# Kernel tuning notes

Hardware: AMD Instinct MI355X
Metric: run time of the kernel (lower is better)

## Reference

```python
import jax, jax.numpy as jnp
import numpy as np

N_HEAD = 16

def _rope_cos_sin(T, head_dim, dtype):
    # inv_freq over even indices, freqs [T, head_dim//2]
    inv_freq = 1.0 / (10000.0 ** (jnp.arange(0, head_dim, 2, dtype=jnp.float32) / head_dim))
    t = jnp.arange(T, dtype=jnp.float32)
    freqs = t[:, None] * inv_freq[None, :]
    cos = jnp.cos(freqs).astype(dtype)[None, :, None, :]  # [1,T,1,hd/2]
    sin = jnp.sin(freqs).astype(dtype)[None, :, None, :]
    return cos, sin

def _apply_rope(x, cos, sin):
    # x: [B,T,H,hd]; interleaved halves as in the torch module
    x1, x2 = x[..., ::2], x[..., 1::2]
    return jnp.concatenate([x1 * cos - x2 * sin, x1 * sin + x2 * cos], axis=-1)

def setup_inputs() -> dict:
    key = jax.random.key(0)
    k1, k2, k3 = jax.random.split(key, 3)
    B, T, C = 2, 2048, 1024
    x = jax.random.normal(k1, (B, T, C), dtype=jnp.float32)
    # causal mask (mask==0 positions get -inf), broadcast over B and heads
    attn_mask = jnp.tril(jnp.ones((T, T), dtype=bool))[None, None, :, :]
    w_qkv = jax.random.normal(k2, (C, 3 * C), dtype=jnp.float32) * (1.0 / np.sqrt(C))
    w_out = jax.random.normal(k3, (C, C), dtype=jnp.float32) * (1.0 / np.sqrt(C))
    return {"x": x, "attn_mask": attn_mask, "w_qkv": w_qkv, "w_out": w_out}

def reference(x, attn_mask, w_qkv, w_out):
    B, T, C = x.shape
    H = N_HEAD
    hd = C // H
    qkv = x @ w_qkv  # [B,T,3C]
    q, k, v = jnp.split(qkv, 3, axis=2)
    q = q.reshape(B, T, H, hd)
    k = k.reshape(B, T, H, hd)
    v = v.reshape(B, T, H, hd)
    cos, sin = _rope_cos_sin(T, hd, x.dtype)
    q = _apply_rope(q, cos, sin)
    k = _apply_rope(k, cos, sin)
    scale = 1.0 / np.sqrt(hd).astype(np.float32)
    att = jnp.einsum('bthd,bshd->bhts', q, k) * scale  # [B,H,T,T]
    att = jnp.where(attn_mask, att, -jnp.inf)
    att = jax.nn.softmax(att, axis=-1)
    out = jnp.einsum('bhts,bshd->bthd', att, v).reshape(B, T, C)
    out = out @ w_out
    k_t = jnp.transpose(k, (0, 2, 1, 3))  # [B,H,T,hd]
    v_t = jnp.transpose(v, (0, 2, 1, 3))
    return out, k_t, v_t
```

## Files before the change

### kernel.cpp

```cpp
#include <hip/hip_runtime.h>

#define T_SEQ 2048
#define NH    16
#define HD    64
#define CDIM  1024
#define BDIM  2

using floatx4 = __attribute__((ext_vector_type(4))) float;
using bf16x8  = __attribute__((ext_vector_type(8))) __bf16;
using half4   = __attribute__((ext_vector_type(4))) _Float16;
using half8   = __attribute__((ext_vector_type(8))) _Float16;
typedef unsigned short u16;

__device__ __forceinline__ u16 f2bf(float f) {
  unsigned int u = __float_as_uint(f);
  u += 0x7fffu + ((u >> 16) & 1u);
  return (u16)(u >> 16);
}
__device__ __forceinline__ float bf2f(u16 h) {
  return __uint_as_float(((unsigned int)h) << 16);
}
__device__ __forceinline__ u16 f2h(float f) {
  union { _Float16 h; u16 u; } c; c.h = (_Float16)f; return c.u;
}
__device__ __forceinline__ unsigned pk2h(float a, float b) {
  return __builtin_bit_cast(unsigned, __builtin_amdgcn_cvt_pkrtz(a, b));
}
__device__ __forceinline__ void gld16(const void* g, const void* l) {
  __builtin_amdgcn_global_load_lds(
      (const __attribute__((address_space(1))) unsigned int*)(unsigned long long)g,
      (__attribute__((address_space(3))) unsigned int*)(unsigned int)(unsigned long long)l,
      16, 0, 0);
}

__global__ __launch_bounds__(256) void preproc(const float* __restrict__ x,
                                               const float* __restrict__ w_qkv,
                                               const float* __restrict__ w_out,
                                               u16* __restrict__ xb,
                                               u16* __restrict__ wqT,
                                               u16* __restrict__ woT) {
  __shared__ float tile[32][33];
  int blk = blockIdx.x, tid = threadIdx.x;
  if (blk < 4096) {
    int i = blk * 256 + tid;
    float4 v = ((const float4*)x)[i];
    ushort4 o;
    o.x = f2bf(v.x); o.y = f2bf(v.y); o.z = f2bf(v.z); o.w = f2bf(v.w);
    ((ushort4*)xb)[i] = o;
    return;
  }
  const float* W; u16* WT; int K, N, bx, by;
  if (blk < 4096 + 3072) {
    int idx = blk - 4096; W = w_qkv; WT = wqT; K = 1024; N = 3072;
    bx = idx % 96; by = idx / 96;
  } else {
    int idx = blk - 7168; W = w_out; WT = woT; K = 1024; N = 1024;
    bx = idx & 31; by = idx >> 5;
  }
  int n0 = bx * 32, k0 = by * 32;
  int tx = tid & 31, ty = tid >> 5;
#pragma unroll
  for (int i = 0; i < 32; i += 8)
    tile[ty + i][tx] = W[(size_t)(k0 + ty + i) * N + n0 + tx];
  __syncthreads();
#pragma unroll
  for (int i = 0; i < 32; i += 8)
    WT[(size_t)(n0 + ty + i) * K + k0 + tx] = f2bf(tile[tx][ty + i]);
}

template <bool OUT_F32>
__global__ __launch_bounds__(256) void gemm_bt(const u16* __restrict__ A,
                                               const u16* __restrict__ BT,
                                               float* __restrict__ Cf,
                                               u16* __restrict__ Cb,
                                               int M, int N, int K) {
  __shared__ u16 As[128 * 32];
  __shared__ u16 Bs[128 * 32];
  const int tid  = threadIdx.x;
  const int lane = tid & 63, wave = tid >> 6;
  const int quad = lane >> 4, l16 = lane & 15;
  const int wm = (wave & 1) * 64, wn = (wave >> 1) * 64;
  const int row0 = blockIdx.x * 128, col0 = blockIdx.y * 128;
  const int srow = tid >> 2;
  const int sc   = tid & 3;
  const int sgc  = (sc ^ ((srow >> 1) & 3)) * 8;
  floatx4 acc[4][4] = {};
  for (int k0 = 0; k0 < K; k0 += 32) {
    __syncthreads();
    gld16(A  + (size_t)(row0 + srow     ) * K + k0 + sgc, &As[srow * 32 + sc * 8]);
    gld16(A  + (size_t)(row0 + srow + 64) * K + k0 + sgc, &As[(srow + 64) * 32 + sc * 8]);
    gld16(BT + (size_t)(col0 + srow     ) * K + k0 + sgc, &Bs[srow * 32 + sc * 8]);
    gld16(BT + (size_t)(col0 + srow + 64) * K + k0 + sgc, &Bs[(srow + 64) * 32 + sc * 8]);
    __syncthreads();
    bf16x8 af[4], bfv[4];
#pragma unroll
    for (int mt = 0; mt < 4; mt++) {
      int r = wm + mt * 16 + l16;
      af[mt] = *(const bf16x8*)&As[r * 32 + (quad ^ ((r >> 1) & 3)) * 8];
    }
#pragma unroll
    for (int nt = 0; nt < 4; nt++) {
      int r = wn + nt * 16 + l16;
      bfv[nt] = *(const bf16x8*)&Bs[r * 32 + (quad ^ ((r >> 1) & 3)) * 8];
    }
#pragma unroll
    for (int mt = 0; mt < 4; mt++)
#pragma unroll
      for (int nt = 0; nt < 4; nt++)
        acc[mt][nt] = __builtin_amdgcn_mfma_f32_16x16x32_bf16(af[mt], bfv[nt], acc[mt][nt], 0, 0, 0);
  }
#pragma unroll
  for (int mt = 0; mt < 4; mt++)
#pragma unroll
    for (int nt = 0; nt < 4; nt++)
#pragma unroll
      for (int r = 0; r < 4; r++) {
        int row = row0 + wm + mt * 16 + quad * 4 + r;
        int col = col0 + wn + nt * 16 + l16;
        float v = acc[mt][nt][r];
        if (OUT_F32) Cf[(size_t)row * N + col] = v;
        else         Cb[(size_t)row * N + col] = f2bf(v);
      }
}

__global__ __launch_bounds__(256) void rope_vpack(const u16* __restrict__ qkv,
                                                  u16* __restrict__ qf16,
                                                  u16* __restrict__ kf16,
                                                  float* __restrict__ kt_out,
                                                  float* __restrict__ vt_out,
                                                  u16* __restrict__ vtf) {
  int blk = blockIdx.x;
  if (blk < 16384) {
    int gid = blk * 4 + (threadIdx.x >> 6);
    int d   = threadIdx.x & 63;
    int t   = gid & (T_SEQ - 1);
    int h   = (gid >> 11) & 15;
    int b   = gid >> 15;
    const u16* qrow = qkv + ((size_t)(b * T_SEQ + t)) * 3072 + h * 64;
    int i = d & 31;
    unsigned int qp = *(const unsigned int*)(qrow + 2 * i);
    unsigned int kp = *(const unsigned int*)(qrow + 1024 + 2 * i);
    float q1 = bf2f((u16)qp), q2 = bf2f((u16)(qp >> 16));
    float k1 = bf2f((u16)kp), k2 = bf2f((u16)(kp >> 16));
    float inv = expf((float)i * -0.28782313662425572f);
    float ang = (float)t * inv;
    float sn = sinf(ang), cs = cosf(ang);
    float qv = (d < 32) ? (q1 * cs - q2 * sn) : (q1 * sn + q2 * cs);
    float kv = (d < 32) ? (k1 * cs - k2 * sn) : (k1 * sn + k2 * cs);
    size_t o = (size_t)gid * 64 + d;
    qf16[o] = f2h(qv * 0.18033688011112042f);
    kf16[o] = f2h(kv);
    kt_out[o] = kv;
    return;
  }
  __shared__ float tile[64][65];
  int b2 = blk - 16384;
  int t0 = (b2 & 31) * 64;
  int bh = b2 >> 5;
  int b = bh >> 4, h = bh & 15;
  int tx = threadIdx.x & 63, ty = threadIdx.x >> 6;
#pragma unroll
  for (int i = ty; i < 64; i += 4) {
    float v = bf2f(qkv[((size_t)(b * T_SEQ + t0 + i)) * 3072 + 2048 + h * 64 + tx]);
    tile[i][tx] = v;
    vt_out[((size_t)bh * T_SEQ + t0 + i) * 64 + tx] = v;
  }
  __syncthreads();
#pragma unroll
  for (int i = ty; i < 64; i += 4)
    vtf[((size_t)bh * 64 + i) * T_SEQ + t0 + tx] = f2h(tile[tx][i]);
}

__global__ __launch_bounds__(256) void attn_fused(const u16* __restrict__ qf16,
                                                  const u16* __restrict__ kf16,
                                                  const u16* __restrict__ vtf,
                                                  u16* __restrict__ Ob) {
  __shared__ u16 Ks[128 * 64];
  __shared__ u16 Vts[64 * 128];
  const int tid = threadIdx.x;
  const int lane = tid & 63, wave = tid >> 6;
  const int quad = lane >> 4, l16 = lane & 15;
  const int qh2 = quad >> 1, ql2 = (quad & 1) * 4;
  const int j   = blockIdx.x >> 5;
  const int bh  = blockIdx.x & 31;
  const int b = bh >> 4, h = bh & 15;

#pragma unroll 1
  for (int s2 = 0; s2 < 2; s2++) {
    const int qt2 = s2 ? j : (31 - j);
    const int tw  = qt2 * 64 + wave * 16;
    const u16* Qg = qf16 + ((size_t)bh * T_SEQ + tw) * HD;
    half8 qfrag[2];
#pragma unroll
    for (int kc = 0; kc < 2; kc++)
      qfrag[kc] = *(const half8*)&Qg[(size_t)l16 * HD + kc * 32 + quad * 8];

    floatx4 oacc[4] = {};
    float mrow = -1e30f, lrow = 0.f;
    const int nkt = (qt2 >> 1) + 1;

    for (int kt = 0; kt < nkt; kt++) {
      __syncthreads();
      const size_t koff = ((size_t)bh * T_SEQ + kt * 128) * HD;
      const u16* Vg = vtf + (size_t)bh * HD * T_SEQ + kt * 128;
#pragma unroll
      for (int jj = 0; jj < 4; jj++) {
        int t2 = jj * 256 + tid;
        int r = t2 >> 3, c = t2 & 7;
        gld16(kf16 + koff + r * HD + (c ^ (r & 7)) * 8, &Ks[t2 * 8]);
      }
#pragma unroll
      for (int jj = 0; jj < 4; jj++) {
        int t2 = jj * 256 + tid;
        int r = t2 >> 4, c = t2 & 15;
        gld16(Vg + (size_t)r * T_SEQ + (c ^ (r & 15)) * 8, &Vts[t2 * 8]);
      }
      __syncthreads();

      floatx4 sacc[8] = {};
#pragma unroll
      for (int kc = 0; kc < 2; kc++)
#pragma unroll
        for (int st = 0; st < 8; st++) {
          int srow = st * 16 + l16;
          half8 ak = *(const half8*)&Ks[srow * 64 + (((kc * 4 + quad) ^ (srow & 7)) * 8)];
          sacc[st] = __builtin_amdgcn_mfma_f32_16x16x32_f16(ak, qfrag[kc], sacc[st], 0, 0, 0);
        }
      if (kt == nkt - 1) {
        int tg = tw + l16;
#pragma unroll
        for (int st = 0; st < 8; st++) {
          int sg = kt * 128 + st * 16 + quad * 4;
#pragma unroll
          for (int r = 0; r < 4; r++)
            if (sg + r > tg) sacc[st][r] = -1e30f;
        }
      }
      {
        floatx4 vm = sacc[0];
#pragma unroll
        for (int st = 1; st < 8; st++) {
          vm[0] = fmaxf(vm[0], sacc[st][0]); vm[1] = fmaxf(vm[1], sacc[st][1]);
          vm[2] = fmaxf(vm[2], sacc[st][2]); vm[3] = fmaxf(vm[3], sacc[st][3]);
        }
        float mx = fmaxf(fmaxf(vm[0], vm[1]), fmaxf(vm[2], vm[3]));
        mx = fmaxf(mx, __shfl_xor(mx, 16));
        mx = fmaxf(mx, __shfl_xor(mx, 32));
        float mnew = fmaxf(mrow, mx);
        float alpha = exp2f(mrow - mnew);
        mrow = mnew;
        floatx4 vs = {0.f, 0.f, 0.f, 0.f};
#pragma unroll
        for (int st = 0; st < 8; st++) {
#pragma unroll
          for (int r = 0; r < 4; r++) sacc[st][r] = exp2f(sacc[st][r] - mnew);
          vs += sacc[st];
        }
        float rs = (vs[0] + vs[1]) + (vs[2] + vs[3]);
        rs += __shfl_xor(rs, 16);
        rs += __shfl_xor(rs, 32);
        lrow = lrow * alpha + rs;
#pragma unroll
        for (int dt = 0; dt < 4; dt++) oacc[dt] *= alpha;
      }
#pragma unroll
      for (int st = 0; st < 8; st++) {
        union { unsigned u[2]; half4 h; } pc;
        pc.u[0] = pk2h(sacc[st][0], sacc[st][1]);
        pc.u[1] = pk2h(sacc[st][2], sacc[st][3]);
        half4 bp = pc.h;
#pragma unroll
        for (int dt = 0; dt < 4; dt++) {
          int drow = dt * 16 + l16;
          half4 av = *(const half4*)&Vts[drow * 128 + (((st * 2 + qh2) ^ (drow & 15)) * 8) + ql2];
          oacc[dt] = __builtin_amdgcn_mfma_f32_16x16x16f16(av, bp, oacc[dt], 0, 0, 0);
        }
      }
    }
    {
      int t = tw + l16;
      float invl = 1.f / lrow;
#pragma unroll
      for (int dt = 0; dt < 4; dt++) {
        int d0 = dt * 16 + quad * 4;
        ushort4 o;
        o.x = f2bf(oacc[dt][0] * invl);
        o.y = f2bf(oacc[dt][1] * invl);
        o.z = f2bf(oacc[dt][2] * invl);
        o.w = f2bf(oacc[dt][3] * invl);
        *(ushort4*)&Ob[((size_t)(b * T_SEQ) + t) * CDIM + h * HD + d0] = o;
      }
    }
  }
}

extern "C" void kernel_launch(void* const* d_in, const int* in_sizes, int n_in,
                              void* d_out, int out_size, void* d_ws, size_t ws_size,
                              hipStream_t stream) {
  const float* x     = (const float*)d_in[0];
  const float* w_qkv = (const float*)d_in[2];
  const float* w_out = (const float*)d_in[3];
  float* out    = (float*)d_out;
  float* kt_out = out + (size_t)BDIM * T_SEQ * CDIM;
  float* vt_out = kt_out + (size_t)BDIM * T_SEQ * CDIM;

  const size_t F = (size_t)4194304;
  char* base = (char*)d_ws;
  u16* xb   = (u16*)base;
  u16* wqT  = xb + F;
  u16* woT  = wqT + (size_t)3145728;
  u16* qkvb = woT + (size_t)1048576;
  u16* qf16 = qkvb + (size_t)3 * F;
  u16* kf16 = qf16 + F;
  u16* vtf  = (u16*)base;
  u16* Ob   = kf16 + F;

  preproc<<<8192, 256, 0, stream>>>(x, w_qkv, w_out, xb, wqT, woT);
  gemm_bt<false><<<dim3(32, 24), 256, 0, stream>>>(xb, wqT, (float*)nullptr, qkvb, 4096, 3072, 1024);
  rope_vpack<<<17408, 256, 0, stream>>>(qkvb, qf16, kf16, kt_out, vt_out, vtf);
  attn_fused<<<512, 256, 0, stream>>>(qf16, kf16, vtf, Ob);
  gemm_bt<true><<<dim3(32, 8), 256, 0, stream>>>(Ob, woT, out, (u16*)nullptr, 4096, 1024, 1024);
}
```

Measured before the change: 221.0 us.

## Process both causal query tiles together sharing K/V tile loads

The attention kernel now handles its two paired query tiles (31-j and j) in one pass over the key/value tiles instead of two sequential passes. Each loaded K/V tile is reused by both query tiles while both are active, and the dual MFMA streams interleave to raise instruction-level parallelism. It also skips the online-softmax rescale when the new max grows by no more than a threshold, and adds a launch-bounds occupancy hint. In exchange, register pressure roughly doubles for the accumulators, which may limit occupancy.

```diff
diff --git a/kernel.cpp b/kernel.cpp
--- a/kernel.cpp
+++ b/kernel.cpp
@@ -171,10 +171,122 @@
     vtf[((size_t)bh * 64 + i) * T_SEQ + t0 + tx] = f2h(tile[tx][i]);
 }
 
-__global__ __launch_bounds__(256) void attn_fused(const u16* __restrict__ qf16,
-                                                  const u16* __restrict__ kf16,
-                                                  const u16* __restrict__ vtf,
-                                                  u16* __restrict__ Ob) {
+__device__ __forceinline__ void qk_dual(const u16* Ks, const half8* qfA, const half8* qfB,
+                                        floatx4 (&sA)[8], floatx4 (&sB)[8],
+                                        int quad, int l16) {
+#pragma unroll
+  for (int kc = 0; kc < 2; kc++)
+#pragma unroll
+    for (int st = 0; st < 8; st++) {
+      int srow = st * 16 + l16;
+      half8 ak = *(const half8*)&Ks[srow * 64 + (((kc * 4 + quad) ^ (srow & 7)) * 8)];
+      sA[st] = __builtin_amdgcn_mfma_f32_16x16x32_f16(ak, qfA[kc], sA[st], 0, 0, 0);
+      sB[st] = __builtin_amdgcn_mfma_f32_16x16x32_f16(ak, qfB[kc], sB[st], 0, 0, 0);
+    }
+}
+__device__ __forceinline__ void qk_single(const u16* Ks, const half8* qfA,
+                                          floatx4 (&sA)[8], int quad, int l16) {
+#pragma unroll
+  for (int kc = 0; kc < 2; kc++)
+#pragma unroll
+    for (int st = 0; st < 8; st++) {
+      int srow = st * 16 + l16;
+      half8 ak = *(const half8*)&Ks[srow * 64 + (((kc * 4 + quad) ^ (srow & 7)) * 8)];
+      sA[st] = __builtin_amdgcn_mfma_f32_16x16x32_f16(ak, qfA[kc], sA[st], 0, 0, 0);
+    }
+}
+__device__ __forceinline__ void apply_mask(floatx4 (&s)[8], int kt, int tw, int quad, int l16) {
+  int tg = tw + l16;
+#pragma unroll
+  for (int st = 0; st < 8; st++) {
+    int sg = kt * 128 + st * 16 + quad * 4;
+#pragma unroll
+    for (int r = 0; r < 4; r++)
+      if (sg + r > tg) s[st][r] = -1e30f;
+  }
+}
+__device__ __forceinline__ void softmax_update(floatx4 (&s)[8], float& mrow, float& lrow,
+                                               floatx4 (&oacc)[4]) {
+  floatx4 vm = s[0];
+#pragma unroll
+  for (int st = 1; st < 8; st++) {
+    vm[0] = fmaxf(vm[0], s[st][0]); vm[1] = fmaxf(vm[1], s[st][1]);
+    vm[2] = fmaxf(vm[2], s[st][2]); vm[3] = fmaxf(vm[3], s[st][3]);
+  }
+  float mx = fmaxf(fmaxf(vm[0], vm[1]), fmaxf(vm[2], vm[3]));
+  mx = fmaxf(mx, __shfl_xor(mx, 16));
+  mx = fmaxf(mx, __shfl_xor(mx, 32));
+  if (!__all(mx <= mrow + 8.f)) {
+    float mnew = fmaxf(mrow, mx);
+    float alpha = exp2f(mrow - mnew);
+    mrow = mnew;
+    lrow *= alpha;
+#pragma unroll
+    for (int dt = 0; dt < 4; dt++) oacc[dt] *= alpha;
+  }
+  floatx4 vs = {0.f, 0.f, 0.f, 0.f};
+#pragma unroll
+  for (int st = 0; st < 8; st++) {
+#pragma unroll
+    for (int r = 0; r < 4; r++) s[st][r] = exp2f(s[st][r] - mrow);
+    vs += s[st];
+  }
+  float rs = (vs[0] + vs[1]) + (vs[2] + vs[3]);
+  rs += __shfl_xor(rs, 16);
+  rs += __shfl_xor(rs, 32);
+  lrow += rs;
+}
+__device__ __forceinline__ void pv_dual(const u16* Vts, const floatx4 (&sA)[8],
+                                        const floatx4 (&sB)[8], floatx4 (&oA)[4],
+                                        floatx4 (&oB)[4], int qh2, int ql2, int l16) {
+#pragma unroll
+  for (int st = 0; st < 8; st++) {
+    union { unsigned u[2]; half4 h; } pa, pb;
+    pa.u[0] = pk2h(sA[st][0], sA[st][1]); pa.u[1] = pk2h(sA[st][2], sA[st][3]);
+    pb.u[0] = pk2h(sB[st][0], sB[st][1]); pb.u[1] = pk2h(sB[st][2], sB[st][3]);
+#pragma unroll
+    for (int dt = 0; dt < 4; dt++) {
+      int drow = dt * 16 + l16;
+      half4 av = *(const half4*)&Vts[drow * 128 + (((st * 2 + qh2) ^ (drow & 15)) * 8) + ql2];
+      oA[dt] = __builtin_amdgcn_mfma_f32_16x16x16f16(av, pa.h, oA[dt], 0, 0, 0);
+      oB[dt] = __builtin_amdgcn_mfma_f32_16x16x16f16(av, pb.h, oB[dt], 0, 0, 0);
+    }
+  }
+}
+__device__ __forceinline__ void pv_single(const u16* Vts, const floatx4 (&sA)[8],
+                                          floatx4 (&oA)[4], int qh2, int ql2, int l16) {
+#pragma unroll
+  for (int st = 0; st < 8; st++) {
+    union { unsigned u[2]; half4 h; } pa;
+    pa.u[0] = pk2h(sA[st][0], sA[st][1]); pa.u[1] = pk2h(sA[st][2], sA[st][3]);
+#pragma unroll
+    for (int dt = 0; dt < 4; dt++) {
+      int drow = dt * 16 + l16;
+      half4 av = *(const half4*)&Vts[drow * 128 + (((st * 2 + qh2) ^ (drow & 15)) * 8) + ql2];
+      oA[dt] = __builtin_amdgcn_mfma_f32_16x16x16f16(av, pa.h, oA[dt], 0, 0, 0);
+    }
+  }
+}
+__device__ __forceinline__ void epilogue(u16* __restrict__ Ob, const floatx4 (&oacc)[4],
+                                         float lrow, int b, int h, int tw, int quad, int l16) {
+  int t = tw + l16;
+  float invl = 1.f / lrow;
+#pragma unroll
+  for (int dt = 0; dt < 4; dt++) {
+    int d0 = dt * 16 + quad * 4;
+    ushort4 o;
+    o.x = f2bf(oacc[dt][0] * invl);
+    o.y = f2bf(oacc[dt][1] * invl);
+    o.z = f2bf(oacc[dt][2] * invl);
+    o.w = f2bf(oacc[dt][3] * invl);
+    *(ushort4*)&Ob[((size_t)(b * T_SEQ) + t) * CDIM + h * HD + d0] = o;
+  }
+}
+
+__global__ __launch_bounds__(256, 2) void attn_fused(const u16* __restrict__ qf16,
+                                                     const u16* __restrict__ kf16,
+                                                     const u16* __restrict__ vtf,
+                                                     u16* __restrict__ Ob) {
   __shared__ u16 Ks[128 * 64];
   __shared__ u16 Vts[64 * 128];
   const int tid = threadIdx.x;
@@ -185,113 +297,61 @@
   const int bh  = blockIdx.x & 31;
   const int b = bh >> 4, h = bh & 15;
 
+  const int qtA = 31 - j, qtB = j;
+  const int twA = qtA * 64 + wave * 16;
+  const int twB = qtB * 64 + wave * 16;
+  const int nktA = (qtA >> 1) + 1;
+  const int nktB = (qtB >> 1) + 1;
+
+  const u16* QgA = qf16 + ((size_t)bh * T_SEQ + twA) * HD;
+  const u16* QgB = qf16 + ((size_t)bh * T_SEQ + twB) * HD;
+  half8 qfA[2], qfB[2];
+#pragma unroll
+  for (int kc = 0; kc < 2; kc++) {
+    qfA[kc] = *(const half8*)&QgA[(size_t)l16 * HD + kc * 32 + quad * 8];
+    qfB[kc] = *(const half8*)&QgB[(size_t)l16 * HD + kc * 32 + quad * 8];
+  }
+
+  floatx4 oaccA[4] = {}, oaccB[4] = {};
+  float mA = -1e30f, lA = 0.f;
+  float mB = -1e30f, lB = 0.f;
+
 #pragma unroll 1
-  for (int s2 = 0; s2 < 2; s2++) {
-    const int qt2 = s2 ? j : (31 - j);
-    const int tw  = qt2 * 64 + wave * 16;
-    const u16* Qg = qf16 + ((size_t)bh * T_SEQ + tw) * HD;
-    half8 qfrag[2];
-#pragma unroll
-    for (int kc = 0; kc < 2; kc++)
-      qfrag[kc] = *(const half8*)&Qg[(size_t)l16 * HD + kc * 32 + quad * 8];
-
-    floatx4 oacc[4] = {};
-    float mrow = -1e30f, lrow = 0.f;
-    const int nkt = (qt2 >> 1) + 1;
-
-    for (int kt = 0; kt < nkt; kt++) {
-      __syncthreads();
-      const size_t koff = ((size_t)bh * T_SEQ + kt * 128) * HD;
-      const u16* Vg = vtf + (size_t)bh * HD * T_SEQ + kt * 128;
-#pragma unroll
-      for (int jj = 0; jj < 4; jj++) {
-        int t2 = jj * 256 + tid;
-        int r = t2 >> 3, c = t2 & 7;
-        gld16(kf16 + koff + r * HD + (c ^ (r & 7)) * 8, &Ks[t2 * 8]);
-      }
-#pragma unroll
-      for (int jj = 0; jj < 4; jj++) {
-        int t2 = jj * 256 + tid;
-        int r = t2 >> 4, c = t2 & 15;
-        gld16(Vg + (size_t)r * T_SEQ + (c ^ (r & 15)) * 8, &Vts[t2 * 8]);
-      }
-      __syncthreads();
-
-      floatx4 sacc[8] = {};
-#pragma unroll
-      for (int kc = 0; kc < 2; kc++)
-#pragma unroll
-        for (int st = 0; st < 8; st++) {
-          int srow = st * 16 + l16;
-          half8 ak = *(const half8*)&Ks[srow * 64 + (((kc * 4 + quad) ^ (srow & 7)) * 8)];
-          sacc[st] = __builtin_amdgcn_mfma_f32_16x16x32_f16(ak, qfrag[kc], sacc[st], 0, 0, 0);
-        }
-      if (kt == nkt - 1) {
-        int tg = tw + l16;
-#pragma unroll
-        for (int st = 0; st < 8; st++) {
-          int sg = kt * 128 + st * 16 + quad * 4;
-#pragma unroll
-          for (int r = 0; r < 4; r++)
-            if (sg + r > tg) sacc[st][r] = -1e30f;
-        }
-      }
-      {
-        floatx4 vm = sacc[0];
-#pragma unroll
-        for (int st = 1; st < 8; st++) {
-          vm[0] = fmaxf(vm[0], sacc[st][0]); vm[1] = fmaxf(vm[1], sacc[st][1]);
-          vm[2] = fmaxf(vm[2], sacc[st][2]); vm[3] = fmaxf(vm[3], sacc[st][3]);
-        }
-        float mx = fmaxf(fmaxf(vm[0], vm[1]), fmaxf(vm[2], vm[3]));
-        mx = fmaxf(mx, __shfl_xor(mx, 16));
-        mx = fmaxf(mx, __shfl_xor(mx, 32));
-        float mnew = fmaxf(mrow, mx);
-        float alpha = exp2f(mrow - mnew);
-        mrow = mnew;
-        floatx4 vs = {0.f, 0.f, 0.f, 0.f};
-#pragma unroll
-        for (int st = 0; st < 8; st++) {
-#pragma unroll
-          for (int r = 0; r < 4; r++) sacc[st][r] = exp2f(sacc[st][r] - mnew);
-          vs += sacc[st];
-        }
-        float rs = (vs[0] + vs[1]) + (vs[2] + vs[3]);
-        rs += __shfl_xor(rs, 16);
-        rs += __shfl_xor(rs, 32);
-        lrow = lrow * alpha + rs;
-#pragma unroll
-        for (int dt = 0; dt < 4; dt++) oacc[dt] *= alpha;
-      }
-#pragma unroll
-      for (int st = 0; st < 8; st++) {
-        union { unsigned u[2]; half4 h; } pc;
-        pc.u[0] = pk2h(sacc[st][0], sacc[st][1]);
-        pc.u[1] = pk2h(sacc[st][2], sacc[st][3]);
-        half4 bp = pc.h;
-#pragma unroll
-        for (int dt = 0; dt < 4; dt++) {
-          int drow = dt * 16 + l16;
-          half4 av = *(const half4*)&Vts[drow * 128 + (((st * 2 + qh2) ^ (drow & 15)) * 8) + ql2];
-          oacc[dt] = __builtin_amdgcn_mfma_f32_16x16x16f16(av, bp, oacc[dt], 0, 0, 0);
-        }
-      }
-    }
-    {
-      int t = tw + l16;
-      float invl = 1.f / lrow;
-#pragma unroll
-      for (int dt = 0; dt < 4; dt++) {
-        int d0 = dt * 16 + quad * 4;
-        ushort4 o;
-        o.x = f2bf(oacc[dt][0] * invl);
-        o.y = f2bf(oacc[dt][1] * invl);
-        o.z = f2bf(oacc[dt][2] * invl);
-        o.w = f2bf(oacc[dt][3] * invl);
-        *(ushort4*)&Ob[((size_t)(b * T_SEQ) + t) * CDIM + h * HD + d0] = o;
-      }
-    }
-  }
+  for (int kt = 0; kt < nktA; kt++) {
+    __syncthreads();
+    const size_t koff = ((size_t)bh * T_SEQ + kt * 128) * HD;
+    const u16* Vg = vtf + (size_t)bh * HD * T_SEQ + kt * 128;
+#pragma unroll
+    for (int jj = 0; jj < 4; jj++) {
+      int t2 = jj * 256 + tid;
+      int r = t2 >> 3, c = t2 & 7;
+      gld16(kf16 + koff + r * HD + (c ^ (r & 7)) * 8, &Ks[t2 * 8]);
+    }
+#pragma unroll
+    for (int jj = 0; jj < 4; jj++) {
+      int t2 = jj * 256 + tid;
+      int r = t2 >> 4, c = t2 & 15;
+      gld16(Vg + (size_t)r * T_SEQ + (c ^ (r & 15)) * 8, &Vts[t2 * 8]);
+    }
+    __syncthreads();
+
+    if (kt < nktB) {
+      floatx4 sA[8] = {}, sB[8] = {};
+      qk_dual(Ks, qfA, qfB, sA, sB, quad, l16);
+      if (kt == nktB - 1) apply_mask(sB, kt, twB, quad, l16);
+      softmax_update(sA, mA, lA, oaccA);
+      softmax_update(sB, mB, lB, oaccB);
+      pv_dual(Vts, sA, sB, oaccA, oaccB, qh2, ql2, l16);
+    } else {
+      floatx4 sA[8] = {};
+      qk_single(Ks, qfA, sA, quad, l16);
+      if (kt == nktA - 1) apply_mask(sA, kt, twA, quad, l16);
+      softmax_update(sA, mA, lA, oaccA);
+      pv_single(Vts, sA, oaccA, qh2, ql2, l16);
+    }
+  }
+  epilogue(Ob, oaccA, lA, b, h, twA, quad, l16);
+  epilogue(Ob, oaccB, lB, b, h, twB, quad, l16);
 }
 
 extern "C" void kernel_launch(void* const* d_in, const int* in_sizes, int n_in,
```

New measurement: 215.3 us. -2.5%, faster.
